# Performance work log

Hardware: AMD Instinct MI355X
Metric: run time of the kernel (lower is better)

The kernel has to match this reference:

```python
import jax, jax.numpy as jnp
import numpy as np

B, S, H, FFN, E = 4, 2048, 2048, 1024, 8


def setup_inputs() -> dict:
    key = jax.random.key(0)
    k0, k1, k2, k3 = jax.random.split(key, 4)
    return {
        "hidden_states": jax.random.normal(k0, (B, S, H), dtype=jnp.float32),
        "gate_w": jax.random.normal(k1, (E, H), dtype=jnp.float32) * 0.02,
        "w13": jax.random.normal(k2, (E, 2 * FFN, H), dtype=jnp.float32) * 0.02,  # [E, 2F, H] (w1 | w3)
        "w2": jax.random.normal(k3, (E, H, FFN), dtype=jnp.float32) * 0.02,        # [E, H, F]
        "top_k": 2,
    }


def reference(hidden_states, gate_w, w13, w2, top_k):
    b, s, h = hidden_states.shape
    num_experts = gate_w.shape[0]
    x = hidden_states.reshape(-1, h)                       # [T, H]
    router_logits = x @ gate_w.T                           # [T, E]
    probs = jax.nn.softmax(router_logits.astype(jnp.float32), axis=-1)
    routing_weights, selected_experts = jax.lax.top_k(probs, top_k)  # [T, K]
    routing_weights = routing_weights / routing_weights.sum(axis=-1, keepdims=True)
    routing_weights = routing_weights.astype(x.dtype)
    out = jnp.zeros_like(x)
    # small fixed loop over experts; intermediates stay [T, 2F] per expert
    for e in range(num_experts):
        h13 = x @ w13[e].T                                 # [T, 2F]
        g, u = jnp.split(h13, 2, axis=-1)
        y = (jax.nn.silu(g) * u) @ w2[e].T                 # [T, H]
        coef = jnp.sum(jnp.where(selected_experts == e, routing_weights, 0.0), axis=-1)
        out = out + coef[:, None] * y
    return out.reshape(b, s, h), router_logits
```

## Files before the change

kernel.cpp:

```cpp
#include <hip/hip_runtime.h>
#include <stdint.h>

typedef short short8 __attribute__((ext_vector_type(8)));
typedef float f32x4 __attribute__((ext_vector_type(4)));
typedef unsigned short u16;

#define T_TOK 8192
#define HID   2048
#define FFNW  1024
#define NE    8
#define NPAIR (2 * T_TOK)

#define VMCNT(n) asm volatile("s_waitcnt vmcnt(" #n ")" ::: "memory")
#define BAR() __builtin_amdgcn_s_barrier()

__device__ __forceinline__ unsigned short f2bf(float f) {
  unsigned int b = __float_as_uint(f);
  b += 0x7fffu + ((b >> 16) & 1u);
  return (unsigned short)(b >> 16);
}
__device__ __forceinline__ float bf2f(unsigned short u) {
  return __uint_as_float(((unsigned)u) << 16);
}

#define GLOAD16(gptr, lptr)                                                          \
  __builtin_amdgcn_global_load_lds(                                                  \
      (const __attribute__((address_space(1))) unsigned int*)(gptr),                 \
      (__attribute__((address_space(3))) unsigned int*)(lptr), 16, 0, 0)

__global__ __launch_bounds__(256) void k_cast(const float* __restrict__ in,
                                              unsigned short* __restrict__ out,
                                              long n8) {
  long i = (long)blockIdx.x * blockDim.x + threadIdx.x;
  long stride = (long)gridDim.x * blockDim.x;
  for (; i < n8; i += stride) {
    const float4* p = (const float4*)(in + i * 8);
    float4 a = p[0], b = p[1];
    uint4 o;
    o.x = (unsigned)f2bf(a.x) | ((unsigned)f2bf(a.y) << 16);
    o.y = (unsigned)f2bf(a.z) | ((unsigned)f2bf(a.w) << 16);
    o.z = (unsigned)f2bf(b.x) | ((unsigned)f2bf(b.y) << 16);
    o.w = (unsigned)f2bf(b.z) | ((unsigned)f2bf(b.w) << 16);
    ((uint4*)out)[i] = o;
  }
}

__global__ __launch_bounds__(256) void k_router(const float* __restrict__ x,
                                                const float* __restrict__ gw,
                                                unsigned short* __restrict__ xb,
                                                float* __restrict__ logits,
                                                int* __restrict__ sel,
                                                float* __restrict__ cw) {
  int wid = threadIdx.x >> 6, lane = threadIdx.x & 63;
  int t = blockIdx.x * 4 + wid;
  const float4* xr = (const float4*)(x + (size_t)t * HID);
  float acc[NE];
#pragma unroll
  for (int e = 0; e < NE; e++) acc[e] = 0.f;
  for (int i = lane; i < HID / 4; i += 64) {
    float4 xv = xr[i];
    ushort4 o;
    o.x = f2bf(xv.x); o.y = f2bf(xv.y); o.z = f2bf(xv.z); o.w = f2bf(xv.w);
    *(ushort4*)(xb + (size_t)t * HID + i * 4) = o;
#pragma unroll
    for (int e = 0; e < NE; e++) {
      float4 gv = ((const float4*)(gw + (size_t)e * HID))[i];
      acc[e] += xv.x * gv.x + xv.y * gv.y + xv.z * gv.z + xv.w * gv.w;
    }
  }
#pragma unroll
  for (int e = 0; e < NE; e++)
    for (int off = 32; off; off >>= 1) acc[e] += __shfl_down(acc[e], off);
  if (lane == 0) {
    float mx = acc[0];
#pragma unroll
    for (int e = 1; e < NE; e++) mx = fmaxf(mx, acc[e]);
    float p[NE];
#pragma unroll
    for (int e = 0; e < NE; e++) p[e] = expf(acc[e] - mx);
    int i1 = 0; float b1 = p[0];
#pragma unroll
    for (int e = 1; e < NE; e++) if (p[e] > b1) { b1 = p[e]; i1 = e; }
    int i2 = -1; float b2 = -1.f;
#pragma unroll
    for (int e = 0; e < NE; e++) if (e != i1 && p[e] > b2) { b2 = p[e]; i2 = e; }
    float denom = b1 + b2;
#pragma unroll
    for (int e = 0; e < NE; e++) logits[(size_t)t * NE + e] = acc[e];
    sel[2 * t] = i1; sel[2 * t + 1] = i2;
    cw[2 * t] = b1 / denom; cw[2 * t + 1] = b2 / denom;
  }
}

__global__ __launch_bounds__(256) void k_count(const int* __restrict__ sel,
                                               u16* __restrict__ lrank,
                                               int* __restrict__ blkcnt) {
  int blk = blockIdx.x, tid = threadIdx.x;
  int t = blk * 256 + tid;
  int e0 = sel[2 * t], e1 = sel[2 * t + 1];
  int wave = tid >> 6, lane = tid & 63;
  unsigned long long below = (1ull << lane) - 1ull;

  int r0 = 0, r1 = 0, c0[NE], c1[NE];
#pragma unroll
  for (int e = 0; e < NE; e++) {
    unsigned long long m = __ballot(e0 == e);
    if (e == e0) r0 = __popcll(m & below);
    c0[e] = __popcll(m);
  }
#pragma unroll
  for (int e = 0; e < NE; e++) {
    unsigned long long m = __ballot(e1 == e);
    if (e == e1) r1 = __popcll(m & below);
    c1[e] = __popcll(m);
  }

  __shared__ int wcnt[4][NE];
  if (lane < NE) wcnt[wave][lane] = c0[lane] + c1[lane];
  __syncthreads();

  int pre0 = 0, pre1 = 0;
  for (int w = 0; w < wave; w++) { pre0 += wcnt[w][e0]; pre1 += wcnt[w][e1]; }
  lrank[2 * t]     = (u16)(pre0 + r0);
  lrank[2 * t + 1] = (u16)(pre1 + c0[e1] + r1);

  if (tid < NE) {
    int s = 0;
    for (int w = 0; w < 4; w++) s += wcnt[w][tid];
    blkcnt[blk * NE + tid] = s;
  }
}

__global__ __launch_bounds__(256) void k_scanplace(const int* __restrict__ sel,
                                                   const u16* __restrict__ lrank,
                                                   const int* __restrict__ blkcnt,
                                                   int* __restrict__ tokc,
                                                   int* __restrict__ inv,
                                                   int* __restrict__ counts,
                                                   int* __restrict__ base_) {
  int blk = blockIdx.x, tid = threadIdx.x;
  __shared__ int s_pre[NE], s_tot[NE], s_base[NE + 1];
  if (tid < NE) {
    int run = 0, tot = 0;
    for (int b = 0; b < 32; b++) {
      int c = blkcnt[b * NE + tid];
      if (b < blk) run += c;
      tot += c;
    }
    s_pre[tid] = run;
    s_tot[tid] = tot;
  }
  __syncthreads();
  if (tid == 0) {
    int a = 0;
    for (int e = 0; e < NE; e++) { s_base[e] = a; a += s_tot[e]; }
    s_base[NE] = a;
  }
  __syncthreads();

  int t = blk * 256 + tid;
#pragma unroll
  for (int k = 0; k < 2; k++) {
    int e = sel[2 * t + k];
    int pos = s_base[e] + s_pre[e] + (int)lrank[2 * t + k];
    tokc[pos] = t;
    inv[2 * t + k] = pos;
  }
  if (blk == 0 && tid < NE) {
    counts[tid] = s_tot[tid];
    base_[tid] = s_base[tid];
  }
}

__device__ __forceinline__ int xcd_remap(int L, int nwg) {
  return (L & 7) * (nwg >> 3) + (L >> 3);
}

template<bool FUSED, int KD, int ND>
__global__ __launch_bounds__(512, 2) void k_gemm(const u16* __restrict__ A,
                                                 const u16* __restrict__ W,
                                                 u16* __restrict__ Y,
                                                 const int* __restrict__ counts,
                                                 const int* __restrict__ base_,
                                                 const int* __restrict__ tokc) {
  int Wk = xcd_remap(blockIdx.x, 2048);
  int by = Wk & 7, bx = (Wk >> 3) & 31, e = Wk >> 8;

  int cnt = counts[e];
  int m0 = bx * 256;
  if (m0 >= cnt) return;
  constexpr int NCOL = FUSED ? 128 : 256;
  int n0 = by * NCOL;
  int bs = base_[e];

  __shared__ u16 lds[2 * 32768];

  int tid = threadIdx.x;
  int wave = tid >> 6, lane = tid & 63;
  int qrow = tid >> 3;
  int cph = tid & 7;

  const u16* wb = W + (size_t)e * (FUSED ? (2 * FFNW) * HID : HID * FFNW);

  size_t aoffU[2][2], boffU[2][2];
  unsigned adst[2][2], bdst[2][2];
#pragma unroll
  for (int u = 0; u < 2; u++) {
#pragma unroll
    for (int j = 0; j < 2; j++) {
      int rA = qrow + u * 64 + j * 128;
      int clogA = cph ^ (rA & 7);
      int slA = m0 + rA;
      int grA;
      if (FUSED) grA = tokc[bs + (slA < cnt ? slA : 0)];
      else       grA = bs + (slA < cnt ? slA : 0);
      aoffU[u][j] = (size_t)grA * KD + (size_t)clogA * 8;
      adst[u][j] = (unsigned)(rA * 64 + cph * 8);
      int rB;
      if (FUSED) rB = qrow + u * 128 + j * 64;
      else       rB = (qrow >> 5) * 64 + (qrow & 31) + u * 32 + j * 128;
      int clogB = cph ^ (rB & 7);
      int grB = FUSED ? (rB < 128 ? n0 + rB : FFNW + n0 + (rB - 128)) : (n0 + rB);
      boffU[u][j] = (size_t)grB * KD + (size_t)clogB * 8;
      bdst[u][j] = (unsigned)(16384 + rB * 64 + cph * 8);
    }
  }

  f32x4 acc[8][4];
#pragma unroll
  for (int mi = 0; mi < 8; mi++)
#pragma unroll
    for (int n = 0; n < 4; n++) acc[mi][n] = (f32x4)(0.f);

  int wm = wave >> 2, wn = wave & 3;
  int arow = wm * 128;
  int frow = lane & 15, fk = lane >> 4;
  int sw[2];
  sw[0] = ((fk) ^ (frow & 7)) << 4;
  sw[1] = ((fk + 4) ^ (frow & 7)) << 4;

  constexpr int NT = KD / 64;

#define STAGE_A(u, Ts)                                                                 \
  {                                                                                    \
    unsigned db = ((unsigned)(Ts) & 1) * 32768;                                        \
    size_t ko = (size_t)(Ts) * 64;                                                     \
    GLOAD16(A + aoffU[u][0] + ko, &lds[db + adst[u][0]]);                              \
    GLOAD16(A + aoffU[u][1] + ko, &lds[db + adst[u][1]]);                              \
  }
#define STAGE_B(u, Ts)                                                                 \
  {                                                                                    \
    unsigned db = ((unsigned)(Ts) & 1) * 32768;                                        \
    size_t ko = (size_t)(Ts) * 64;                                                     \
    GLOAD16(wb + boffU[u][0] + ko, &lds[db + bdst[u][0]]);                             \
    GLOAD16(wb + boffU[u][1] + ko, &lds[db + bdst[u][1]]);                             \
  }

  STAGE_A(0, 0); STAGE_B(0, 0); STAGE_A(1, 0); STAGE_B(1, 0);
  STAGE_A(0, 1); STAGE_B(0, 1);
  VMCNT(4);
  BAR();

  short8 af[4][2], bn0[2][2], bn1[2][2];

  for (int T = 0; T < NT; ++T) {
    const char* sb = (const char*)lds + ((unsigned)(T & 1)) * 65536;

#pragma unroll
    for (int mi = 0; mi < 4; mi++)
#pragma unroll
      for (int kk = 0; kk < 2; kk++)
        af[mi][kk] = *(const short8*)(sb + (arow + mi * 16 + frow) * 128 + sw[kk]);
#pragma unroll
    for (int n = 0; n < 2; n++) {
      int rb = FUSED ? (wn * 32 + n * 16 + frow) : (wn * 64 + n * 16 + frow);
#pragma unroll
      for (int kk = 0; kk < 2; kk++)
        bn0[n][kk] = *(const short8*)(sb + 65536 / 2 + rb * 128 + sw[kk]);
    }
    if (T + 1 < NT) STAGE_A(1, T + 1);
    BAR();
    __builtin_amdgcn_s_setprio(1);
#pragma unroll
    for (int mi = 0; mi < 4; mi++)
#pragma unroll
      for (int n = 0; n < 2; n++)
#pragma unroll
        for (int kk = 0; kk < 2; kk++)
          acc[mi][n] = __builtin_amdgcn_mfma_f32_16x16x32_bf16(af[mi][kk], bn0[n][kk], acc[mi][n], 0, 0, 0);
    __builtin_amdgcn_s_setprio(0);
    BAR();

#pragma unroll
    for (int n = 0; n < 2; n++) {
      int rb = FUSED ? (128 + wn * 32 + n * 16 + frow) : (wn * 64 + 32 + n * 16 + frow);
#pragma unroll
      for (int kk = 0; kk < 2; kk++)
        bn1[n][kk] = *(const short8*)(sb + 65536 / 2 + rb * 128 + sw[kk]);
    }
    if (T + 1 < NT) STAGE_B(1, T + 1);
    BAR();
    __builtin_amdgcn_s_setprio(1);
#pragma unroll
    for (int mi = 0; mi < 4; mi++)
#pragma unroll
      for (int n = 0; n < 2; n++)
#pragma unroll
        for (int kk = 0; kk < 2; kk++)
          acc[mi][n + 2] = __builtin_amdgcn_mfma_f32_16x16x32_bf16(af[mi][kk], bn1[n][kk], acc[mi][n + 2], 0, 0, 0);
    __builtin_amdgcn_s_setprio(0);
    BAR();

#pragma unroll
    for (int mi = 0; mi < 4; mi++)
#pragma unroll
      for (int kk = 0; kk < 2; kk++)
        af[mi][kk] = *(const short8*)(sb + (arow + 64 + mi * 16 + frow) * 128 + sw[kk]);
    if (T + 2 < NT) STAGE_A(0, T + 2);
    BAR();
    __builtin_amdgcn_s_setprio(1);
#pragma unroll
    for (int mi = 0; mi < 4; mi++)
#pragma unroll
      for (int n = 0; n < 2; n++)
#pragma unroll
        for (int kk = 0; kk < 2; kk++)
          acc[mi + 4][n] = __builtin_amdgcn_mfma_f32_16x16x32_bf16(af[mi][kk], bn0[n][kk], acc[mi + 4][n], 0, 0, 0);
    __builtin_amdgcn_s_setprio(0);
    BAR();

    if (T + 2 < NT) STAGE_B(0, T + 2);
    BAR();
    __builtin_amdgcn_s_setprio(1);
#pragma unroll
    for (int mi = 0; mi < 4; mi++)
#pragma unroll
      for (int n = 0; n < 2; n++)
#pragma unroll
        for (int kk = 0; kk < 2; kk++)
          acc[mi + 4][n + 2] = __builtin_amdgcn_mfma_f32_16x16x32_bf16(af[mi][kk], bn1[n][kk], acc[mi + 4][n + 2], 0, 0, 0);
    __builtin_amdgcn_s_setprio(0);
    if (T < NT - 2) { VMCNT(4); }
    else if (T == NT - 2) { VMCNT(0); }
    BAR();
  }
#undef STAGE_A
#undef STAGE_B

#pragma unroll
  for (int mi = 0; mi < 8; mi++) {
#pragma unroll
    for (int r = 0; r < 4; r++) {
      int row = arow + mi * 16 + fk * 4 + r;
      int sl = m0 + row;
      if (sl < cnt) {
        if (FUSED) {
          u16* yr = Y + (size_t)(bs + sl) * ND + n0 + wn * 32 + frow;
#pragma unroll
          for (int j = 0; j < 2; j++) {
            float g = acc[mi][j][r];
            float u = acc[mi][j + 2][r];
            float sv = g / (1.f + expf(-g));
            yr[j * 16] = f2bf(sv * u);
          }
        } else {
          u16* yr = Y + (size_t)(bs + sl) * ND + n0 + wn * 64 + frow;
#pragma unroll
          for (int n = 0; n < 4; n++) yr[n * 16] = f2bf(acc[mi][n][r]);
        }
      }
    }
  }
}

__global__ __launch_bounds__(256) void k_combine(const unsigned short* __restrict__ y,
                                                 const int* __restrict__ inv,
                                                 const float* __restrict__ cw,
                                                 float* __restrict__ out) {
  long i = (long)blockIdx.x * 256 + threadIdx.x;
  int t = (int)(i >> 8);
  int c = (int)(i & 255);
  int p0 = inv[2 * t], p1 = inv[2 * t + 1];
  float c0 = cw[2 * t], c1 = cw[2 * t + 1];
  short8 y0 = *(const short8*)(y + (size_t)p0 * HID + c * 8);
  short8 y1 = *(const short8*)(y + (size_t)p1 * HID + c * 8);
  float4 o0, o1;
  o0.x = c0 * bf2f((unsigned short)y0[0]) + c1 * bf2f((unsigned short)y1[0]);
  o0.y = c0 * bf2f((unsigned short)y0[1]) + c1 * bf2f((unsigned short)y1[1]);
  o0.z = c0 * bf2f((unsigned short)y0[2]) + c1 * bf2f((unsigned short)y1[2]);
  o0.w = c0 * bf2f((unsigned short)y0[3]) + c1 * bf2f((unsigned short)y1[3]);
  o1.x = c0 * bf2f((unsigned short)y0[4]) + c1 * bf2f((unsigned short)y1[4]);
  o1.y = c0 * bf2f((unsigned short)y0[5]) + c1 * bf2f((unsigned short)y1[5]);
  o1.z = c0 * bf2f((unsigned short)y0[6]) + c1 * bf2f((unsigned short)y1[6]);
  o1.w = c0 * bf2f((unsigned short)y0[7]) + c1 * bf2f((unsigned short)y1[7]);
  float4* op = (float4*)(out + (size_t)t * HID + c * 8);
  op[0] = o0;
  op[1] = o1;
}

extern "C" void kernel_launch(void* const* d_in, const int* in_sizes, int n_in,
                              void* d_out, int out_size, void* d_ws, size_t ws_size,
                              hipStream_t stream) {
  const float* x   = (const float*)d_in[0];
  const float* gw  = (const float*)d_in[1];
  const float* w13 = (const float*)d_in[2];
  const float* w2  = (const float*)d_in[3];
  float* out = (float*)d_out;
  float* logits = out + (size_t)T_TOK * HID;

  uint8_t* p = (uint8_t*)d_ws;
  unsigned short* xb   = (unsigned short*)p; p += (size_t)T_TOK * HID * 2;
  unsigned short* w13b = (unsigned short*)p; p += (size_t)NE * 2 * FFNW * HID * 2;
  unsigned short* w2b  = (unsigned short*)p; p += (size_t)NE * HID * FFNW * 2;
  unsigned short* act  = (unsigned short*)p; p += (size_t)NPAIR * FFNW * 2;
  unsigned short* y    = (unsigned short*)p; p += (size_t)NPAIR * HID * 2;
  int* sel  = (int*)p;   p += (size_t)NPAIR * 4;
  float* cw = (float*)p; p += (size_t)NPAIR * 4;
  int* tokc = (int*)p;   p += (size_t)NPAIR * 4;
  int* inv  = (int*)p;   p += (size_t)NPAIR * 4;
  u16* lrank = (u16*)p;  p += (size_t)NPAIR * 2;
  int* blkcnt = (int*)p; p += 32 * NE * 4;
  int* counts = (int*)p; p += 256;
  int* base   = (int*)p; p += 256;
  if ((size_t)(p - (uint8_t*)d_ws) > ws_size) return;

  k_cast<<<2048, 256, 0, stream>>>(w13, w13b, (long)NE * 2 * FFNW * HID / 8);
  k_cast<<<2048, 256, 0, stream>>>(w2, w2b, (long)NE * HID * FFNW / 8);
  k_router<<<T_TOK / 4, 256, 0, stream>>>(x, gw, xb, logits, sel, cw);
  k_count<<<32, 256, 0, stream>>>(sel, lrank, blkcnt);
  k_scanplace<<<32, 256, 0, stream>>>(sel, lrank, blkcnt, tokc, inv, counts, base);

  k_gemm<true, HID, FFNW><<<2048, 512, 0, stream>>>(xb, w13b, act, counts, base, tokc);
  k_gemm<false, FFNW, HID><<<2048, 512, 0, stream>>>(act, w2b, y, counts, base, tokc);
  k_combine<<<(int)((long)T_TOK * HID / 8 / 256), 256, 0, stream>>>(y, inv, cw, out);
}
```

Measured before the change: 386.9 us.

## Switch grouped MoE GEMMs to persistent grid over compacted tile list

Replaces the fixed 2048-block grid, in which most blocks exit early because their expert has few tokens, with a persistent 512-block grid. Each block loops over a compacted list of valid (expert, m-tile, n-tile) work items built from per-expert tile prefix sums computed in the scan kernel. This removes launch and scheduling cost for empty blocks and balances work across CUs. The cost is serialized tile processing inside each block with no overlap between items, a per-item expert lookup, and a possible tail imbalance.

```diff
diff --git a/kernel.cpp b/kernel.cpp
--- a/kernel.cpp
+++ b/kernel.cpp
@@ -137,7 +137,8 @@
                                                    int* __restrict__ tokc,
                                                    int* __restrict__ inv,
                                                    int* __restrict__ counts,
-                                                   int* __restrict__ base_) {
+                                                   int* __restrict__ base_,
+                                                   int* __restrict__ mpre) {
   int blk = blockIdx.x, tid = threadIdx.x;
   __shared__ int s_pre[NE], s_tot[NE], s_base[NE + 1];
   if (tid < NE) {
@@ -166,9 +167,16 @@
     tokc[pos] = t;
     inv[2 * t + k] = pos;
   }
-  if (blk == 0 && tid < NE) {
-    counts[tid] = s_tot[tid];
-    base_[tid] = s_base[tid];
+  if (blk == 0) {
+    if (tid < NE) {
+      counts[tid] = s_tot[tid];
+      base_[tid] = s_base[tid];
+    }
+    if (tid == 0) {
+      int a = 0;
+      for (int e = 0; e < NE; e++) { mpre[e] = a; a += (s_tot[e] + 255) >> 8; }
+      mpre[NE] = a;
+    }
   }
 }
 
@@ -182,55 +190,36 @@
                                                  u16* __restrict__ Y,
                                                  const int* __restrict__ counts,
                                                  const int* __restrict__ base_,
-                                                 const int* __restrict__ tokc) {
-  int Wk = xcd_remap(blockIdx.x, 2048);
-  int by = Wk & 7, bx = (Wk >> 3) & 31, e = Wk >> 8;
-
-  int cnt = counts[e];
-  int m0 = bx * 256;
-  if (m0 >= cnt) return;
+                                                 const int* __restrict__ tokc,
+                                                 const int* __restrict__ mpre) {
+  int bid = xcd_remap(blockIdx.x, 512);
   constexpr int NCOL = FUSED ? 128 : 256;
-  int n0 = by * NCOL;
-  int bs = base_[e];
-
-  __shared__ u16 lds[2 * 32768];
+
+  int mp[NE + 1];
+#pragma unroll
+  for (int k = 0; k <= NE; k++) mp[k] = mpre[k];
+  int NI = mp[NE] * 8;
 
   int tid = threadIdx.x;
   int wave = tid >> 6, lane = tid & 63;
   int qrow = tid >> 3;
   int cph = tid & 7;
 
-  const u16* wb = W + (size_t)e * (FUSED ? (2 * FFNW) * HID : HID * FFNW);
-
-  size_t aoffU[2][2], boffU[2][2];
   unsigned adst[2][2], bdst[2][2];
+  int rBl[2][2];
 #pragma unroll
   for (int u = 0; u < 2; u++) {
 #pragma unroll
     for (int j = 0; j < 2; j++) {
       int rA = qrow + u * 64 + j * 128;
-      int clogA = cph ^ (rA & 7);
-      int slA = m0 + rA;
-      int grA;
-      if (FUSED) grA = tokc[bs + (slA < cnt ? slA : 0)];
-      else       grA = bs + (slA < cnt ? slA : 0);
-      aoffU[u][j] = (size_t)grA * KD + (size_t)clogA * 8;
       adst[u][j] = (unsigned)(rA * 64 + cph * 8);
       int rB;
       if (FUSED) rB = qrow + u * 128 + j * 64;
       else       rB = (qrow >> 5) * 64 + (qrow & 31) + u * 32 + j * 128;
-      int clogB = cph ^ (rB & 7);
-      int grB = FUSED ? (rB < 128 ? n0 + rB : FFNW + n0 + (rB - 128)) : (n0 + rB);
-      boffU[u][j] = (size_t)grB * KD + (size_t)clogB * 8;
+      rBl[u][j] = rB;
       bdst[u][j] = (unsigned)(16384 + rB * 64 + cph * 8);
     }
   }
-
-  f32x4 acc[8][4];
-#pragma unroll
-  for (int mi = 0; mi < 8; mi++)
-#pragma unroll
-    for (int n = 0; n < 4; n++) acc[mi][n] = (f32x4)(0.f);
 
   int wm = wave >> 2, wn = wave & 3;
   int arow = wm * 128;
@@ -241,132 +230,173 @@
 
   constexpr int NT = KD / 64;
 
+  __shared__ u16 lds[2 * 32768];
+
+  for (int item = bid; item < NI; item += 512) {
+    int e = NE - 1;
+#pragma unroll
+    for (int k = NE - 1; k >= 1; k--)
+      if (item < mp[k] * 8) e = k - 1;
+    int local = item - mp[e] * 8;
+    int m0 = (local >> 3) * 256;
+    int n0 = (local & 7) * NCOL;
+    int cnt = counts[e];
+    int bs = base_[e];
+
+    const u16* wb = W + (size_t)e * (FUSED ? (2 * FFNW) * HID : HID * FFNW);
+
+    size_t aoffU[2][2], boffU[2][2];
+#pragma unroll
+    for (int u = 0; u < 2; u++) {
+#pragma unroll
+      for (int j = 0; j < 2; j++) {
+        int rA = qrow + u * 64 + j * 128;
+        int clogA = cph ^ (rA & 7);
+        int slA = m0 + rA;
+        int grA;
+        if (FUSED) grA = tokc[bs + (slA < cnt ? slA : 0)];
+        else       grA = bs + (slA < cnt ? slA : 0);
+        aoffU[u][j] = (size_t)grA * KD + (size_t)clogA * 8;
+        int rB = rBl[u][j];
+        int clogB = cph ^ (rB & 7);
+        int grB = FUSED ? (rB < 128 ? n0 + rB : FFNW + n0 + (rB - 128)) : (n0 + rB);
+        boffU[u][j] = (size_t)grB * KD + (size_t)clogB * 8;
+      }
+    }
+
+    f32x4 acc[8][4];
+#pragma unroll
+    for (int mi = 0; mi < 8; mi++)
+#pragma unroll
+      for (int n = 0; n < 4; n++) acc[mi][n] = (f32x4)(0.f);
+
 #define STAGE_A(u, Ts)                                                                 \
-  {                                                                                    \
-    unsigned db = ((unsigned)(Ts) & 1) * 32768;                                        \
-    size_t ko = (size_t)(Ts) * 64;                                                     \
-    GLOAD16(A + aoffU[u][0] + ko, &lds[db + adst[u][0]]);                              \
-    GLOAD16(A + aoffU[u][1] + ko, &lds[db + adst[u][1]]);                              \
-  }
+    {                                                                                  \
+      unsigned db = ((unsigned)(Ts) & 1) * 32768;                                      \
+      size_t ko = (size_t)(Ts) * 64;                                                   \
+      GLOAD16(A + aoffU[u][0] + ko, &lds[db + adst[u][0]]);                            \
+      GLOAD16(A + aoffU[u][1] + ko, &lds[db + adst[u][1]]);                            \
+    }
 #define STAGE_B(u, Ts)                                                                 \
-  {                                                                                    \
-    unsigned db = ((unsigned)(Ts) & 1) * 32768;                                        \
-    size_t ko = (size_t)(Ts) * 64;                                                     \
-    GLOAD16(wb + boffU[u][0] + ko, &lds[db + bdst[u][0]]);                             \
-    GLOAD16(wb + boffU[u][1] + ko, &lds[db + bdst[u][1]]);                             \
-  }
-
-  STAGE_A(0, 0); STAGE_B(0, 0); STAGE_A(1, 0); STAGE_B(1, 0);
-  STAGE_A(0, 1); STAGE_B(0, 1);
-  VMCNT(4);
-  BAR();
-
-  short8 af[4][2], bn0[2][2], bn1[2][2];
-
-  for (int T = 0; T < NT; ++T) {
-    const char* sb = (const char*)lds + ((unsigned)(T & 1)) * 65536;
-
-#pragma unroll
-    for (int mi = 0; mi < 4; mi++)
-#pragma unroll
-      for (int kk = 0; kk < 2; kk++)
-        af[mi][kk] = *(const short8*)(sb + (arow + mi * 16 + frow) * 128 + sw[kk]);
-#pragma unroll
-    for (int n = 0; n < 2; n++) {
-      int rb = FUSED ? (wn * 32 + n * 16 + frow) : (wn * 64 + n * 16 + frow);
-#pragma unroll
-      for (int kk = 0; kk < 2; kk++)
-        bn0[n][kk] = *(const short8*)(sb + 65536 / 2 + rb * 128 + sw[kk]);
-    }
-    if (T + 1 < NT) STAGE_A(1, T + 1);
+    {                                                                                  \
+      unsigned db = ((unsigned)(Ts) & 1) * 32768;                                      \
+      size_t ko = (size_t)(Ts) * 64;                                                   \
+      GLOAD16(wb + boffU[u][0] + ko, &lds[db + bdst[u][0]]);                           \
+      GLOAD16(wb + boffU[u][1] + ko, &lds[db + bdst[u][1]]);                           \
+    }
+
+    STAGE_A(0, 0); STAGE_B(0, 0); STAGE_A(1, 0); STAGE_B(1, 0);
+    STAGE_A(0, 1); STAGE_B(0, 1);
+    VMCNT(4);
     BAR();
-    __builtin_amdgcn_s_setprio(1);
-#pragma unroll
-    for (int mi = 0; mi < 4; mi++)
-#pragma unroll
-      for (int n = 0; n < 2; n++)
+
+    short8 af[4][2], bn0[2][2], bn1[2][2];
+
+    for (int T = 0; T < NT; ++T) {
+      const char* sb = (const char*)lds + ((unsigned)(T & 1)) * 65536;
+
+#pragma unroll
+      for (int mi = 0; mi < 4; mi++)
 #pragma unroll
         for (int kk = 0; kk < 2; kk++)
-          acc[mi][n] = __builtin_amdgcn_mfma_f32_16x16x32_bf16(af[mi][kk], bn0[n][kk], acc[mi][n], 0, 0, 0);
-    __builtin_amdgcn_s_setprio(0);
-    BAR();
-
-#pragma unroll
-    for (int n = 0; n < 2; n++) {
-      int rb = FUSED ? (128 + wn * 32 + n * 16 + frow) : (wn * 64 + 32 + n * 16 + frow);
-#pragma unroll
-      for (int kk = 0; kk < 2; kk++)
-        bn1[n][kk] = *(const short8*)(sb + 65536 / 2 + rb * 128 + sw[kk]);
-    }
-    if (T + 1 < NT) STAGE_B(1, T + 1);
-    BAR();
-    __builtin_amdgcn_s_setprio(1);
-#pragma unroll
-    for (int mi = 0; mi < 4; mi++)
-#pragma unroll
-      for (int n = 0; n < 2; n++)
+          af[mi][kk] = *(const short8*)(sb + (arow + mi * 16 + frow) * 128 + sw[kk]);
+#pragma unroll
+      for (int n = 0; n < 2; n++) {
+        int rb = FUSED ? (wn * 32 + n * 16 + frow) : (wn * 64 + n * 16 + frow);
 #pragma unroll
         for (int kk = 0; kk < 2; kk++)
-          acc[mi][n + 2] = __builtin_amdgcn_mfma_f32_16x16x32_bf16(af[mi][kk], bn1[n][kk], acc[mi][n + 2], 0, 0, 0);
-    __builtin_amdgcn_s_setprio(0);
-    BAR();
-
-#pragma unroll
-    for (int mi = 0; mi < 4; mi++)
-#pragma unroll
-      for (int kk = 0; kk < 2; kk++)
-        af[mi][kk] = *(const short8*)(sb + (arow + 64 + mi * 16 + frow) * 128 + sw[kk]);
-    if (T + 2 < NT) STAGE_A(0, T + 2);
-    BAR();
-    __builtin_amdgcn_s_setprio(1);
-#pragma unroll
-    for (int mi = 0; mi < 4; mi++)
-#pragma unroll
-      for (int n = 0; n < 2; n++)
+          bn0[n][kk] = *(const short8*)(sb + 65536 / 2 + rb * 128 + sw[kk]);
+      }
+      if (T + 1 < NT) STAGE_A(1, T + 1);
+      BAR();
+      __builtin_amdgcn_s_setprio(1);
+#pragma unroll
+      for (int mi = 0; mi < 4; mi++)
+#pragma unroll
+        for (int n = 0; n < 2; n++)
+#pragma unroll
+          for (int kk = 0; kk < 2; kk++)
+            acc[mi][n] = __builtin_amdgcn_mfma_f32_16x16x32_bf16(af[mi][kk], bn0[n][kk], acc[mi][n], 0, 0, 0);
+      __builtin_amdgcn_s_setprio(0);
+      BAR();
+
+#pragma unroll
+      for (int n = 0; n < 2; n++) {
+        int rb = FUSED ? (128 + wn * 32 + n * 16 + frow) : (wn * 64 + 32 + n * 16 + frow);
 #pragma unroll
         for (int kk = 0; kk < 2; kk++)
-          acc[mi + 4][n] = __builtin_amdgcn_mfma_f32_16x16x32_bf16(af[mi][kk], bn0[n][kk], acc[mi + 4][n], 0, 0, 0);
-    __builtin_amdgcn_s_setprio(0);
-    BAR();
-
-    if (T + 2 < NT) STAGE_B(0, T + 2);
-    BAR();
-    __builtin_amdgcn_s_setprio(1);
-#pragma unroll
-    for (int mi = 0; mi < 4; mi++)
-#pragma unroll
-      for (int n = 0; n < 2; n++)
+          bn1[n][kk] = *(const short8*)(sb + 65536 / 2 + rb * 128 + sw[kk]);
+      }
+      if (T + 1 < NT) STAGE_B(1, T + 1);
+      BAR();
+      __builtin_amdgcn_s_setprio(1);
+#pragma unroll
+      for (int mi = 0; mi < 4; mi++)
+#pragma unroll
+        for (int n = 0; n < 2; n++)
+#pragma unroll
+          for (int kk = 0; kk < 2; kk++)
+            acc[mi][n + 2] = __builtin_amdgcn_mfma_f32_16x16x32_bf16(af[mi][kk], bn1[n][kk], acc[mi][n + 2], 0, 0, 0);
+      __builtin_amdgcn_s_setprio(0);
+      BAR();
+
+#pragma unroll
+      for (int mi = 0; mi < 4; mi++)
 #pragma unroll
         for (int kk = 0; kk < 2; kk++)
-          acc[mi + 4][n + 2] = __builtin_amdgcn_mfma_f32_16x16x32_bf16(af[mi][kk], bn1[n][kk], acc[mi + 4][n + 2], 0, 0, 0);
-    __builtin_amdgcn_s_setprio(0);
-    if (T < NT - 2) { VMCNT(4); }
-    else if (T == NT - 2) { VMCNT(0); }
-    BAR();
-  }
+          af[mi][kk] = *(const short8*)(sb + (arow + 64 + mi * 16 + frow) * 128 + sw[kk]);
+      if (T + 2 < NT) STAGE_A(0, T + 2);
+      BAR();
+      __builtin_amdgcn_s_setprio(1);
+#pragma unroll
+      for (int mi = 0; mi < 4; mi++)
+#pragma unroll
+        for (int n = 0; n < 2; n++)
+#pragma unroll
+          for (int kk = 0; kk < 2; kk++)
+            acc[mi + 4][n] = __builtin_amdgcn_mfma_f32_16x16x32_bf16(af[mi][kk], bn0[n][kk], acc[mi + 4][n], 0, 0, 0);
+      __builtin_amdgcn_s_setprio(0);
+      BAR();
+
+      if (T + 2 < NT) STAGE_B(0, T + 2);
+      BAR();
+      __builtin_amdgcn_s_setprio(1);
+#pragma unroll
+      for (int mi = 0; mi < 4; mi++)
+#pragma unroll
+        for (int n = 0; n < 2; n++)
+#pragma unroll
+          for (int kk = 0; kk < 2; kk++)
+            acc[mi + 4][n + 2] = __builtin_amdgcn_mfma_f32_16x16x32_bf16(af[mi][kk], bn1[n][kk], acc[mi + 4][n + 2], 0, 0, 0);
+      __builtin_amdgcn_s_setprio(0);
+      if (T < NT - 2) { VMCNT(4); }
+      else if (T == NT - 2) { VMCNT(0); }
+      BAR();
+    }
 #undef STAGE_A
 #undef STAGE_B
 
 #pragma unroll
-  for (int mi = 0; mi < 8; mi++) {
-#pragma unroll
-    for (int r = 0; r < 4; r++) {
-      int row = arow + mi * 16 + fk * 4 + r;
-      int sl = m0 + row;
-      if (sl < cnt) {
-        if (FUSED) {
-          u16* yr = Y + (size_t)(bs + sl) * ND + n0 + wn * 32 + frow;
-#pragma unroll
-          for (int j = 0; j < 2; j++) {
-            float g = acc[mi][j][r];
-            float u = acc[mi][j + 2][r];
-            float sv = g / (1.f + expf(-g));
-            yr[j * 16] = f2bf(sv * u);
+    for (int mi = 0; mi < 8; mi++) {
+#pragma unroll
+      for (int r = 0; r < 4; r++) {
+        int row = arow + mi * 16 + fk * 4 + r;
+        int sl = m0 + row;
+        if (sl < cnt) {
+          if (FUSED) {
+            u16* yr = Y + (size_t)(bs + sl) * ND + n0 + wn * 32 + frow;
+#pragma unroll
+            for (int j = 0; j < 2; j++) {
+              float g = acc[mi][j][r];
+              float u = acc[mi][j + 2][r];
+              float sv = g / (1.f + expf(-g));
+              yr[j * 16] = f2bf(sv * u);
+            }
+          } else {
+            u16* yr = Y + (size_t)(bs + sl) * ND + n0 + wn * 64 + frow;
+#pragma unroll
+            for (int n = 0; n < 4; n++) yr[n * 16] = f2bf(acc[mi][n][r]);
           }
-        } else {
-          u16* yr = Y + (size_t)(bs + sl) * ND + n0 + wn * 64 + frow;
-#pragma unroll
-          for (int n = 0; n < 4; n++) yr[n * 16] = f2bf(acc[mi][n][r]);
         }
       }
     }
@@ -422,15 +452,16 @@
   int* blkcnt = (int*)p; p += 32 * NE * 4;
   int* counts = (int*)p; p += 256;
   int* base   = (int*)p; p += 256;
+  int* mpre   = (int*)p; p += 256;
   if ((size_t)(p - (uint8_t*)d_ws) > ws_size) return;
 
   k_cast<<<2048, 256, 0, stream>>>(w13, w13b, (long)NE * 2 * FFNW * HID / 8);
   k_cast<<<2048, 256, 0, stream>>>(w2, w2b, (long)NE * HID * FFNW / 8);
   k_router<<<T_TOK / 4, 256, 0, stream>>>(x, gw, xb, logits, sel, cw);
   k_count<<<32, 256, 0, stream>>>(sel, lrank, blkcnt);
-  k_scanplace<<<32, 256, 0, stream>>>(sel, lrank, blkcnt, tokc, inv, counts, base);
-
-  k_gemm<true, HID, FFNW><<<2048, 512, 0, stream>>>(xb, w13b, act, counts, base, tokc);
-  k_gemm<false, FFNW, HID><<<2048, 512, 0, stream>>>(act, w2b, y, counts, base, tokc);
+  k_scanplace<<<32, 256, 0, stream>>>(sel, lrank, blkcnt, tokc, inv, counts, base, mpre);
+
+  k_gemm<true, HID, FFNW><<<512, 512, 0, stream>>>(xb, w13b, act, counts, base, tokc, mpre);
+  k_gemm<false, FFNW, HID><<<512, 512, 0, stream>>>(act, w2b, y, counts, base, tokc, mpre);
   k_combine<<<(int)((long)T_TOK * HID / 8 / 256), 256, 0, stream>>>(y, inv, cw, out);
 }
```

After: 400.5 us. 3.5% more time.
